# Performance work log

Measured on AMD Instinct MI355X. Metric: run time of the kernel, lower is better.

The kernel has to match this reference:

```python
import jax, jax.numpy as jnp
import numpy as np

N_NODES = 100000
N_EDGES = 1600000
F_IN = 128
F_OUT = 64


def setup_inputs() -> dict:
    key = jax.random.key(0)
    k1, k2, k3, k4 = jax.random.split(key, 4)
    node_features = jax.random.normal(k1, (N_NODES, F_IN), dtype=jnp.float32)
    edge_index = jax.random.randint(k2, (2, N_EDGES), 0, N_NODES, dtype=jnp.int32)
    edge_weight = jax.random.uniform(k3, (N_EDGES,), dtype=jnp.float32)
    W = jax.random.normal(k4, (F_IN, F_OUT), dtype=jnp.float32) * (1.0 / np.sqrt(F_IN))
    b = jnp.zeros((F_OUT,), dtype=jnp.float32)
    return {"node_features": node_features, "edge_index": edge_index,
            "edge_weight": edge_weight, "W": W, "b": b}


def reference(node_features, edge_index, edge_weight, W, b):
    # GCNConv: x' = D^{-1/2} (A + I) D^{-1/2} (X W) + b, edge-weighted.
    n = node_features.shape[0]
    row, col = edge_index[0], edge_index[1]  # source, target
    # add self-loops with weight 1
    loop = jnp.arange(n, dtype=edge_index.dtype)
    row_f = jnp.concatenate([row, loop])
    col_f = jnp.concatenate([col, loop])
    w_f = jnp.concatenate([edge_weight, jnp.ones((n,), edge_weight.dtype)])
    # symmetric normalization
    deg = jax.ops.segment_sum(w_f, col_f, num_segments=n)  # [N]
    dis = jnp.where(deg > 0, jax.lax.rsqrt(deg), 0.0)      # deg^{-1/2}
    norm = dis[row_f] * w_f * dis[col_f]                   # [E+N]
    # transform then scatter-aggregate messages at targets
    xw = node_features @ W                                  # [N, F_OUT]
    msgs = norm[:, None] * xw[row_f]                        # [E+N, F_OUT]
    out = jax.ops.segment_sum(msgs, col_f, num_segments=n)  # [N, F_OUT]
    out = out + b
    # ReLU; dropout(p=0.001) is identity in inference mode
    return jax.nn.relu(out)
```

## Files before the change

kernel.cpp:

```cpp
#include <hip/hip_runtime.h>

#define F_IN 128
#define F_OUT 64
#define LSTR 136
#define EB 4096
#define BSH 8
#define BNODES 256
#define RITER 12

typedef __bf16 bf16x8 __attribute__((ext_vector_type(8)));
typedef float f32x4 __attribute__((ext_vector_type(4)));

__device__ inline ushort f2bf(float f) {
    unsigned u = __float_as_uint(f);
    return (ushort)((u + 0x7fff + ((u >> 16) & 1)) >> 16);
}
__device__ inline float bf2f(ushort u) { return __uint_as_float((unsigned)u << 16); }

__global__ __launch_bounds__(256, 8) void k_hist_gemm(
        const float* __restrict__ X, const float* __restrict__ W,
        const int* __restrict__ colp, unsigned* __restrict__ partials,
        ushort* __restrict__ xwb, int n, int e, int nblk, int nbuck) {
    __shared__ unsigned cnt[512];
    __shared__ ushort Wt[64 * LSTR];
    const int t = threadIdx.x;

    if ((int)blockIdx.x < nblk) {
        const int blk = (int)blockIdx.x;
        cnt[t] = 0; cnt[t + 256] = 0;
        __syncthreads();
        const int base = blk * EB;
        #pragma unroll
        for (int j = 0; j < EB / 256; ++j) {
            int i = base + j * 256 + t;
            if (i < e) atomicAdd(&cnt[(unsigned)colp[i] >> BSH], 1u);
        }
        __syncthreads();
        for (int b = t; b < nbuck; b += 256)
            partials[(size_t)b * nblk + blk] = cnt[b];
        return;
    }

    const int row0 = ((int)blockIdx.x - nblk) * 64;
    const float4* W4 = (const float4*)W;
    #pragma unroll
    for (int i = 0; i < 8; ++i) {
        int idx = t + i * 256;
        float4 v = W4[idx];
        int flat = idx * 4;
        int k = flat >> 6, c = flat & 63;
        Wt[(c + 0) * LSTR + k] = f2bf(v.x);
        Wt[(c + 1) * LSTR + k] = f2bf(v.y);
        Wt[(c + 2) * LSTR + k] = f2bf(v.z);
        Wt[(c + 3) * LSTR + k] = f2bf(v.w);
    }
    const int lane = t & 63, wv_ = t >> 6;
    const int m16 = lane & 15, quad = lane >> 4;
    int arow = row0 + wv_ * 16 + m16;
    if (arow >= n) arow = n - 1;
    const float* xr = X + (long)arow * F_IN;
    __syncthreads();

    f32x4 acc[4] = {{0,0,0,0},{0,0,0,0},{0,0,0,0},{0,0,0,0}};
    #pragma unroll
    for (int kk = 0; kk < 4; ++kk) {
        float4 xa = *(const float4*)(xr + kk * 32 + quad * 8);
        float4 xb = *(const float4*)(xr + kk * 32 + quad * 8 + 4);
        union { ushort us[8]; bf16x8 v; } ua;
        ua.us[0] = f2bf(xa.x); ua.us[1] = f2bf(xa.y);
        ua.us[2] = f2bf(xa.z); ua.us[3] = f2bf(xa.w);
        ua.us[4] = f2bf(xb.x); ua.us[5] = f2bf(xb.y);
        ua.us[6] = f2bf(xb.z); ua.us[7] = f2bf(xb.w);
        #pragma unroll
        for (int nt = 0; nt < 4; ++nt) {
            bf16x8 bb = *(const bf16x8*)&Wt[(nt * 16 + m16) * LSTR + kk * 32 + quad * 8];
            acc[nt] = __builtin_amdgcn_mfma_f32_16x16x32_bf16(ua.v, bb, acc[nt], 0, 0, 0);
        }
    }
    #pragma unroll
    for (int nt = 0; nt < 4; ++nt) {
        #pragma unroll
        for (int reg = 0; reg < 4; ++reg) {
            int gr = row0 + wv_ * 16 + quad * 4 + reg;
            if (gr < n) xwb[(long)gr * F_OUT + nt * 16 + m16] = f2bf(acc[nt][reg]);
        }
    }
}

__global__ __launch_bounds__(512) void k_scan_blocks(
        unsigned* __restrict__ partials, unsigned* __restrict__ totals,
        int nblk, int nbuck) {
    __shared__ unsigned s[512];
    const int b = (int)blockIdx.x, t = threadIdx.x;
    unsigned v = (t < nblk) ? partials[(size_t)b * nblk + t] : 0;
    s[t] = v;
    __syncthreads();
    for (int off = 1; off < 512; off <<= 1) {
        unsigned u = (t >= off) ? s[t - off] : 0;
        __syncthreads();
        s[t] += u;
        __syncthreads();
    }
    if (t < nblk) partials[(size_t)b * nblk + t] = s[t] - v;
    if (t == 511) totals[b] = s[511];
}

__global__ __launch_bounds__(512) void k_scatter(
        const int* __restrict__ ei, const float* __restrict__ ew,
        const unsigned* __restrict__ partials, const unsigned* __restrict__ totals,
        unsigned* __restrict__ sortedA, unsigned char* __restrict__ cl,
        int e, int nblk, int nbuck) {
    __shared__ unsigned srt[EB];
    __shared__ unsigned meta[EB];
    __shared__ unsigned s[512];
    __shared__ unsigned cnt[512];
    __shared__ unsigned ptr[512];
    __shared__ unsigned delta[512];
    const int t = threadIdx.x, blk = (int)blockIdx.x;

    unsigned tv = (t < nbuck) ? totals[t] : 0;
    s[t] = tv; cnt[t] = 0;
    __syncthreads();
    for (int off = 1; off < 512; off <<= 1) {
        unsigned u = (t >= off) ? s[t - off] : 0;
        __syncthreads();
        s[t] += u;
        __syncthreads();
    }
    const unsigned bs = s[t] - tv;

    const int base = blk * EB;
    unsigned cc[EB / 512], rr[EB / 512], ww[EB / 512];
    #pragma unroll
    for (int jj = 0; jj < EB / 512; ++jj) {
        int i = base + jj * 512 + t;
        unsigned c = 0xffffffffu, r = 0, w15 = 0;
        if (i < e) {
            c = (unsigned)ei[e + i];
            r = (unsigned)ei[i];
            unsigned u = __float_as_uint(ew[i]);
            w15 = ((u + 0x7fff + ((u >> 16) & 1)) >> 16) & 0x7fffu;
            atomicAdd(&cnt[c >> BSH], 1u);
        }
        cc[jj] = c; rr[jj] = r; ww[jj] = w15;
    }
    __syncthreads();

    unsigned cv = cnt[t];
    s[t] = cv;
    __syncthreads();
    for (int off = 1; off < 512; off <<= 1) {
        unsigned u = (t >= off) ? s[t - off] : 0;
        __syncthreads();
        s[t] += u;
        __syncthreads();
    }
    const unsigned excl = s[t] - cv;
    ptr[t] = excl;
    delta[t] = bs + ((t < nbuck) ? partials[(size_t)t * nblk + blk] : 0) - excl;
    __syncthreads();

    #pragma unroll
    for (int jj = 0; jj < EB / 512; ++jj) {
        if (cc[jj] != 0xffffffffu) {
            unsigned d = atomicAdd(&ptr[cc[jj] >> BSH], 1u);
            srt[d] = (rr[jj] << 15) | ww[jj];
            meta[d] = cc[jj];
        }
    }
    __syncthreads();

    const int cnum = (e - base < EB) ? (e - base) : EB;
    #pragma unroll
    for (int jj = 0; jj < EB / 512; ++jj) {
        int i = jj * 512 + t;
        if (i < cnum) {
            unsigned c = meta[i];
            unsigned dest = delta[c >> BSH] + (unsigned)i;
            sortedA[dest] = srt[i];
            cl[dest] = (unsigned char)(c & (BNODES - 1));
        }
    }
}

__global__ __launch_bounds__(512) void k_sort_deg(
        unsigned* __restrict__ sortedA, const unsigned char* __restrict__ cl,
        const unsigned* __restrict__ totals, unsigned* __restrict__ nbeg,
        float* __restrict__ dis, int n, int e, int nbuck) {
    __shared__ unsigned s[512];
    __shared__ unsigned cnt[BNODES];
    __shared__ unsigned offs[BNODES];
    __shared__ unsigned ptr[BNODES];
    __shared__ float dl[BNODES];
    __shared__ unsigned Sh, Eh;
    const int b = (int)blockIdx.x, t = threadIdx.x;

    unsigned tv = (t < nbuck) ? totals[t] : 0;
    s[t] = tv;
    __syncthreads();
    for (int off = 1; off < 512; off <<= 1) {
        unsigned u = (t >= off) ? s[t - off] : 0;
        __syncthreads();
        s[t] += u;
        __syncthreads();
    }
    if (t == b) { Sh = s[t] - tv; Eh = s[t]; }
    if (t < BNODES) { cnt[t] = 0; dl[t] = 0.f; }
    __syncthreads();
    const unsigned S = Sh;
    const int seg = (int)(Eh - S);

    unsigned rec[RITER];
    unsigned clp[RITER / 4];
    #pragma unroll
    for (int jj = 0; jj < RITER; ++jj) {
        int j = jj * 512 + t;
        unsigned r = 0, c = 0;
        if (j < seg) {
            r = sortedA[S + j];
            c = cl[S + j];
            atomicAdd(&cnt[c], 1u);
            atomicAdd(&dl[c], __uint_as_float((r & 0x7fffu) << 16));
        }
        rec[jj] = r;
        if ((jj & 3) == 0) clp[jj >> 2] = c;
        else               clp[jj >> 2] |= c << ((jj & 3) * 8);
    }
    __syncthreads();
    if (t < BNODES) offs[t] = cnt[t];
    __syncthreads();
    for (int off = 1; off < BNODES; off <<= 1) {
        unsigned u = (t < BNODES && t >= off) ? offs[t - off] : 0;
        __syncthreads();
        if (t < BNODES) offs[t] += u;
        __syncthreads();
    }
    if (t < BNODES) ptr[t] = offs[t] - cnt[t];
    __syncthreads();
    #pragma unroll
    for (int jj = 0; jj < RITER; ++jj) {
        int j = jj * 512 + t;
        if (j < seg) {
            unsigned c = (clp[jj >> 2] >> ((jj & 3) * 8)) & 0xffu;
            unsigned d = atomicAdd(&ptr[c], 1u);
            sortedA[S + d] = rec[jj];
        }
    }
    if (t < BNODES) {
        int c = b * BNODES + t;
        if (c < n) {
            nbeg[c] = S + (offs[t] - cnt[t]);
            dis[c] = rsqrtf(dl[t] + 1.0f);
        }
    }
    if (b == 0 && t == 0) nbeg[n] = (unsigned)e;
}

__global__ __launch_bounds__(256, 8) void k_gather(
        const unsigned* __restrict__ sortedA, const unsigned* __restrict__ nbeg,
        const float* __restrict__ dis, const ushort* __restrict__ xwb,
        const float* __restrict__ bias, float* __restrict__ out, int n) {
    int node = (int)blockIdx.x * 4 + (threadIdx.x >> 6);
    if (node >= n) return;
    int lane = threadIdx.x & 63, q = lane >> 4, fl = lane & 15;
    unsigned bg = nbeg[node], en = nbeg[node + 1];
    if (en < bg) en = bg;
    int beg = (int)bg, end = (int)en;
    float dc = dis[node];
    float a0 = 0.f, a1 = 0.f, a2 = 0.f, a3 = 0.f;
    if (q == 0) {
        ushort4 xv = *(const ushort4*)(xwb + (long)node * 64 + fl * 4);
        a0 = dc * bf2f(xv.x); a1 = dc * bf2f(xv.y);
        a2 = dc * bf2f(xv.z); a3 = dc * bf2f(xv.w);
    }
    int j = beg + q;
    for (; j + 12 < end; j += 16) {
        unsigned v0 = sortedA[j],     v1 = sortedA[j + 4];
        unsigned v2 = sortedA[j + 8], v3 = sortedA[j + 12];
        int r0 = (int)(v0 >> 15), r1 = (int)(v1 >> 15);
        int r2 = (int)(v2 >> 15), r3 = (int)(v3 >> 15);
        float d0 = dis[r0], d1 = dis[r1], d2 = dis[r2], d3 = dis[r3];
        ushort4 x0 = *(const ushort4*)(xwb + (long)r0 * 64 + fl * 4);
        ushort4 x1 = *(const ushort4*)(xwb + (long)r1 * 64 + fl * 4);
        ushort4 x2 = *(const ushort4*)(xwb + (long)r2 * 64 + fl * 4);
        ushort4 x3 = *(const ushort4*)(xwb + (long)r3 * 64 + fl * 4);
        float w0 = __uint_as_float((v0 & 0x7fffu) << 16) * d0;
        float w1 = __uint_as_float((v1 & 0x7fffu) << 16) * d1;
        float w2 = __uint_as_float((v2 & 0x7fffu) << 16) * d2;
        float w3 = __uint_as_float((v3 & 0x7fffu) << 16) * d3;
        a0 += w0 * bf2f(x0.x) + w1 * bf2f(x1.x) + w2 * bf2f(x2.x) + w3 * bf2f(x3.x);
        a1 += w0 * bf2f(x0.y) + w1 * bf2f(x1.y) + w2 * bf2f(x2.y) + w3 * bf2f(x3.y);
        a2 += w0 * bf2f(x0.z) + w1 * bf2f(x1.z) + w2 * bf2f(x2.z) + w3 * bf2f(x3.z);
        a3 += w0 * bf2f(x0.w) + w1 * bf2f(x1.w) + w2 * bf2f(x2.w) + w3 * bf2f(x3.w);
    }
    for (; j < end; j += 4) {
        unsigned v = sortedA[j];
        int r = (int)(v >> 15);
        float w = __uint_as_float((v & 0x7fffu) << 16) * dis[r];
        ushort4 x = *(const ushort4*)(xwb + (long)r * 64 + fl * 4);
        a0 += w * bf2f(x.x); a1 += w * bf2f(x.y);
        a2 += w * bf2f(x.z); a3 += w * bf2f(x.w);
    }
    a0 += __shfl_xor(a0, 16); a0 += __shfl_xor(a0, 32);
    a1 += __shfl_xor(a1, 16); a1 += __shfl_xor(a1, 32);
    a2 += __shfl_xor(a2, 16); a2 += __shfl_xor(a2, 32);
    a3 += __shfl_xor(a3, 16); a3 += __shfl_xor(a3, 32);
    if (q == 0) {
        float4 bb = ((const float4*)bias)[fl];
        float f0 = dc * a0 + bb.x, f1 = dc * a1 + bb.y;
        float f2 = dc * a2 + bb.z, f3 = dc * a3 + bb.w;
        ((float4*)out)[(long)node * 16 + fl] =
            make_float4(f0 > 0.f ? f0 : 0.f, f1 > 0.f ? f1 : 0.f,
                        f2 > 0.f ? f2 : 0.f, f3 > 0.f ? f3 : 0.f);
    }
}

extern "C" void kernel_launch(void* const* d_in, const int* in_sizes, int n_in,
                              void* d_out, int out_size, void* d_ws, size_t ws_size,
                              hipStream_t stream) {
    const float* X  = (const float*)d_in[0];
    const int*   ei = (const int*)d_in[1];
    const float* ew = (const float*)d_in[2];
    const float* W  = (const float*)d_in[3];
    const float* b  = (const float*)d_in[4];
    float* out = (float*)d_out;

    const int n = in_sizes[0] / F_IN;
    const int e = in_sizes[2];

    const int NBLK  = (e + EB - 1) / EB;
    const int NBUCK = (n + BNODES - 1) / BNODES;
    const int nb_gemm = (n + 63) / 64;

    long p = 0;
    auto alloc = [&](long bytes) { long off = p; p += (bytes + 255) & ~255L; return off; };
    char* ws = (char*)d_ws;
    long o_part   = alloc((long)NBUCK * NBLK * 4);
    long o_tot    = alloc((long)NBUCK * 4);
    long o_sorted = alloc((long)e * 4);
    long o_cl     = alloc((long)e);
    long o_dis    = alloc((long)n * 4);
    long o_nbeg   = alloc((long)(n + 1) * 4);
    long o_xwb    = alloc((long)n * F_OUT * 2);
    unsigned*      partials = (unsigned*)(ws + o_part);
    unsigned*      totals   = (unsigned*)(ws + o_tot);
    unsigned*      sortedA  = (unsigned*)(ws + o_sorted);
    unsigned char* cl       = (unsigned char*)(ws + o_cl);
    float*         dis      = (float*)(ws + o_dis);
    unsigned*      nbeg     = (unsigned*)(ws + o_nbeg);
    ushort*        xwb      = (ushort*)(ws + o_xwb);

    k_hist_gemm<<<NBLK + nb_gemm, 256, 0, stream>>>(X, W, ei + e, partials, xwb,
                                                    n, e, NBLK, NBUCK);
    k_scan_blocks<<<NBUCK, 512, 0, stream>>>(partials, totals, NBLK, NBUCK);
    k_scatter<<<NBLK, 512, 0, stream>>>(ei, ew, partials, totals, sortedA, cl,
                                        e, NBLK, NBUCK);
    k_sort_deg<<<NBUCK, 512, 0, stream>>>(sortedA, cl, totals, nbeg, dis,
                                          n, e, NBUCK);
    k_gather<<<(n + 3) / 4, 256, 0, stream>>>(sortedA, nbeg, dis, xwb, b, out, n);
}
```

Before: 203.2 us.

## Move X@W GEMM blocks from histogram kernel into scatter kernel

```diff
diff --git a/kernel.cpp b/kernel.cpp
--- a/kernel.cpp
+++ b/kernel.cpp
@@ -17,74 +17,22 @@
 }
 __device__ inline float bf2f(ushort u) { return __uint_as_float((unsigned)u << 16); }
 
-__global__ __launch_bounds__(256, 8) void k_hist_gemm(
-        const float* __restrict__ X, const float* __restrict__ W,
+__global__ __launch_bounds__(256) void k_hist(
         const int* __restrict__ colp, unsigned* __restrict__ partials,
-        ushort* __restrict__ xwb, int n, int e, int nblk, int nbuck) {
+        int e, int nblk, int nbuck) {
     __shared__ unsigned cnt[512];
-    __shared__ ushort Wt[64 * LSTR];
-    const int t = threadIdx.x;
-
-    if ((int)blockIdx.x < nblk) {
-        const int blk = (int)blockIdx.x;
-        cnt[t] = 0; cnt[t + 256] = 0;
-        __syncthreads();
-        const int base = blk * EB;
-        #pragma unroll
-        for (int j = 0; j < EB / 256; ++j) {
-            int i = base + j * 256 + t;
-            if (i < e) atomicAdd(&cnt[(unsigned)colp[i] >> BSH], 1u);
-        }
-        __syncthreads();
-        for (int b = t; b < nbuck; b += 256)
-            partials[(size_t)b * nblk + blk] = cnt[b];
-        return;
-    }
-
-    const int row0 = ((int)blockIdx.x - nblk) * 64;
-    const float4* W4 = (const float4*)W;
-    #pragma unroll
-    for (int i = 0; i < 8; ++i) {
-        int idx = t + i * 256;
-        float4 v = W4[idx];
-        int flat = idx * 4;
-        int k = flat >> 6, c = flat & 63;
-        Wt[(c + 0) * LSTR + k] = f2bf(v.x);
-        Wt[(c + 1) * LSTR + k] = f2bf(v.y);
-        Wt[(c + 2) * LSTR + k] = f2bf(v.z);
-        Wt[(c + 3) * LSTR + k] = f2bf(v.w);
-    }
-    const int lane = t & 63, wv_ = t >> 6;
-    const int m16 = lane & 15, quad = lane >> 4;
-    int arow = row0 + wv_ * 16 + m16;
-    if (arow >= n) arow = n - 1;
-    const float* xr = X + (long)arow * F_IN;
-    __syncthreads();
-
-    f32x4 acc[4] = {{0,0,0,0},{0,0,0,0},{0,0,0,0},{0,0,0,0}};
-    #pragma unroll
-    for (int kk = 0; kk < 4; ++kk) {
-        float4 xa = *(const float4*)(xr + kk * 32 + quad * 8);
-        float4 xb = *(const float4*)(xr + kk * 32 + quad * 8 + 4);
-        union { ushort us[8]; bf16x8 v; } ua;
-        ua.us[0] = f2bf(xa.x); ua.us[1] = f2bf(xa.y);
-        ua.us[2] = f2bf(xa.z); ua.us[3] = f2bf(xa.w);
-        ua.us[4] = f2bf(xb.x); ua.us[5] = f2bf(xb.y);
-        ua.us[6] = f2bf(xb.z); ua.us[7] = f2bf(xb.w);
-        #pragma unroll
-        for (int nt = 0; nt < 4; ++nt) {
-            bf16x8 bb = *(const bf16x8*)&Wt[(nt * 16 + m16) * LSTR + kk * 32 + quad * 8];
-            acc[nt] = __builtin_amdgcn_mfma_f32_16x16x32_bf16(ua.v, bb, acc[nt], 0, 0, 0);
-        }
-    }
-    #pragma unroll
-    for (int nt = 0; nt < 4; ++nt) {
-        #pragma unroll
-        for (int reg = 0; reg < 4; ++reg) {
-            int gr = row0 + wv_ * 16 + quad * 4 + reg;
-            if (gr < n) xwb[(long)gr * F_OUT + nt * 16 + m16] = f2bf(acc[nt][reg]);
-        }
-    }
+    const int t = threadIdx.x, blk = (int)blockIdx.x;
+    cnt[t] = 0; cnt[t + 256] = 0;
+    __syncthreads();
+    const int base = blk * EB;
+    #pragma unroll
+    for (int j = 0; j < EB / 256; ++j) {
+        int i = base + j * 256 + t;
+        if (i < e) atomicAdd(&cnt[(unsigned)colp[i] >> BSH], 1u);
+    }
+    __syncthreads();
+    for (int b = t; b < nbuck; b += 256)
+        partials[(size_t)b * nblk + blk] = cnt[b];
 }
 
 __global__ __launch_bounds__(512) void k_scan_blocks(
@@ -105,29 +53,85 @@
     if (t == 511) totals[b] = s[511];
 }
 
-__global__ __launch_bounds__(512) void k_scatter(
+__global__ __launch_bounds__(512) void k_scatter_gemm(
+        const float* __restrict__ X, const float* __restrict__ W,
         const int* __restrict__ ei, const float* __restrict__ ew,
         const unsigned* __restrict__ partials, const unsigned* __restrict__ totals,
         unsigned* __restrict__ sortedA, unsigned char* __restrict__ cl,
-        int e, int nblk, int nbuck) {
-    __shared__ unsigned srt[EB];
-    __shared__ unsigned meta[EB];
-    __shared__ unsigned s[512];
-    __shared__ unsigned cnt[512];
-    __shared__ unsigned ptr[512];
-    __shared__ unsigned delta[512];
-    const int t = threadIdx.x, blk = (int)blockIdx.x;
-
+        ushort* __restrict__ xwb, int n, int e, int nblk, int nbuck) {
+    __shared__ union SM {
+        struct {
+            unsigned srt[EB];
+            unsigned meta[EB];
+            unsigned s[512];
+            unsigned cnt[512];
+            unsigned ptr[512];
+            unsigned delta[512];
+        } sc;
+        ushort Wt[64 * LSTR];
+    } sm;
+    const int t = threadIdx.x;
+
+    if ((int)blockIdx.x >= nblk) {
+        ushort* Wt = sm.Wt;
+        const int row0 = ((int)blockIdx.x - nblk) * 128;
+        const float4* W4 = (const float4*)W;
+        #pragma unroll
+        for (int i = 0; i < 4; ++i) {
+            int idx = t + i * 512;
+            float4 v = W4[idx];
+            int flat = idx * 4;
+            int k = flat >> 6, c = flat & 63;
+            Wt[(c + 0) * LSTR + k] = f2bf(v.x);
+            Wt[(c + 1) * LSTR + k] = f2bf(v.y);
+            Wt[(c + 2) * LSTR + k] = f2bf(v.z);
+            Wt[(c + 3) * LSTR + k] = f2bf(v.w);
+        }
+        const int lane = t & 63, wv_ = t >> 6;
+        const int m16 = lane & 15, quad = lane >> 4;
+        int arow = row0 + wv_ * 16 + m16;
+        if (arow >= n) arow = n - 1;
+        const float* xr = X + (long)arow * F_IN;
+        __syncthreads();
+
+        f32x4 acc[4] = {{0,0,0,0},{0,0,0,0},{0,0,0,0},{0,0,0,0}};
+        #pragma unroll
+        for (int kk = 0; kk < 4; ++kk) {
+            float4 xa = *(const float4*)(xr + kk * 32 + quad * 8);
+            float4 xb = *(const float4*)(xr + kk * 32 + quad * 8 + 4);
+            union { ushort us[8]; bf16x8 v; } ua;
+            ua.us[0] = f2bf(xa.x); ua.us[1] = f2bf(xa.y);
+            ua.us[2] = f2bf(xa.z); ua.us[3] = f2bf(xa.w);
+            ua.us[4] = f2bf(xb.x); ua.us[5] = f2bf(xb.y);
+            ua.us[6] = f2bf(xb.z); ua.us[7] = f2bf(xb.w);
+            #pragma unroll
+            for (int nt = 0; nt < 4; ++nt) {
+                bf16x8 bb = *(const bf16x8*)&Wt[(nt * 16 + m16) * LSTR + kk * 32 + quad * 8];
+                acc[nt] = __builtin_amdgcn_mfma_f32_16x16x32_bf16(ua.v, bb, acc[nt], 0, 0, 0);
+            }
+        }
+        #pragma unroll
+        for (int nt = 0; nt < 4; ++nt) {
+            #pragma unroll
+            for (int reg = 0; reg < 4; ++reg) {
+                int gr = row0 + wv_ * 16 + quad * 4 + reg;
+                if (gr < n) xwb[(long)gr * F_OUT + nt * 16 + m16] = f2bf(acc[nt][reg]);
+            }
+        }
+        return;
+    }
+
+    const int blk = (int)blockIdx.x;
     unsigned tv = (t < nbuck) ? totals[t] : 0;
-    s[t] = tv; cnt[t] = 0;
+    sm.sc.s[t] = tv; sm.sc.cnt[t] = 0;
     __syncthreads();
     for (int off = 1; off < 512; off <<= 1) {
-        unsigned u = (t >= off) ? s[t - off] : 0;
-        __syncthreads();
-        s[t] += u;
-        __syncthreads();
-    }
-    const unsigned bs = s[t] - tv;
+        unsigned u = (t >= off) ? sm.sc.s[t - off] : 0;
+        __syncthreads();
+        sm.sc.s[t] += u;
+        __syncthreads();
+    }
+    const unsigned bs = sm.sc.s[t] - tv;
 
     const int base = blk * EB;
     unsigned cc[EB / 512], rr[EB / 512], ww[EB / 512];
@@ -140,32 +144,32 @@
             r = (unsigned)ei[i];
             unsigned u = __float_as_uint(ew[i]);
             w15 = ((u + 0x7fff + ((u >> 16) & 1)) >> 16) & 0x7fffu;
-            atomicAdd(&cnt[c >> BSH], 1u);
+            atomicAdd(&sm.sc.cnt[c >> BSH], 1u);
         }
         cc[jj] = c; rr[jj] = r; ww[jj] = w15;
     }
     __syncthreads();
 
-    unsigned cv = cnt[t];
-    s[t] = cv;
+    unsigned cv = sm.sc.cnt[t];
+    sm.sc.s[t] = cv;
     __syncthreads();
     for (int off = 1; off < 512; off <<= 1) {
-        unsigned u = (t >= off) ? s[t - off] : 0;
-        __syncthreads();
-        s[t] += u;
-        __syncthreads();
-    }
-    const unsigned excl = s[t] - cv;
-    ptr[t] = excl;
-    delta[t] = bs + ((t < nbuck) ? partials[(size_t)t * nblk + blk] : 0) - excl;
+        unsigned u = (t >= off) ? sm.sc.s[t - off] : 0;
+        __syncthreads();
+        sm.sc.s[t] += u;
+        __syncthreads();
+    }
+    const unsigned excl = sm.sc.s[t] - cv;
+    sm.sc.ptr[t] = excl;
+    sm.sc.delta[t] = bs + ((t < nbuck) ? partials[(size_t)t * nblk + blk] : 0) - excl;
     __syncthreads();
 
     #pragma unroll
     for (int jj = 0; jj < EB / 512; ++jj) {
         if (cc[jj] != 0xffffffffu) {
-            unsigned d = atomicAdd(&ptr[cc[jj] >> BSH], 1u);
-            srt[d] = (rr[jj] << 15) | ww[jj];
-            meta[d] = cc[jj];
+            unsigned d = atomicAdd(&sm.sc.ptr[cc[jj] >> BSH], 1u);
+            sm.sc.srt[d] = (rr[jj] << 15) | ww[jj];
+            sm.sc.meta[d] = cc[jj];
         }
     }
     __syncthreads();
@@ -175,9 +179,9 @@
     for (int jj = 0; jj < EB / 512; ++jj) {
         int i = jj * 512 + t;
         if (i < cnum) {
-            unsigned c = meta[i];
-            unsigned dest = delta[c >> BSH] + (unsigned)i;
-            sortedA[dest] = srt[i];
+            unsigned c = sm.sc.meta[i];
+            unsigned dest = sm.sc.delta[c >> BSH] + (unsigned)i;
+            sortedA[dest] = sm.sc.srt[i];
             cl[dest] = (unsigned char)(c & (BNODES - 1));
         }
     }
@@ -273,10 +277,11 @@
         a0 = dc * bf2f(xv.x); a1 = dc * bf2f(xv.y);
         a2 = dc * bf2f(xv.z); a3 = dc * bf2f(xv.w);
     }
-    int j = beg + q;
-    for (; j + 12 < end; j += 16) {
-        unsigned v0 = sortedA[j],     v1 = sortedA[j + 4];
-        unsigned v2 = sortedA[j + 8], v3 = sortedA[j + 12];
+    for (int j = beg + q; j < end; j += 16) {
+        bool m1 = j + 4 < end, m2 = j + 8 < end, m3 = j + 12 < end;
+        int j1 = m1 ? j + 4 : j, j2 = m2 ? j + 8 : j, j3 = m3 ? j + 12 : j;
+        unsigned v0 = sortedA[j],  v1 = sortedA[j1];
+        unsigned v2 = sortedA[j2], v3 = sortedA[j3];
         int r0 = (int)(v0 >> 15), r1 = (int)(v1 >> 15);
         int r2 = (int)(v2 >> 15), r3 = (int)(v3 >> 15);
         float d0 = dis[r0], d1 = dis[r1], d2 = dis[r2], d3 = dis[r3];
@@ -285,21 +290,13 @@
         ushort4 x2 = *(const ushort4*)(xwb + (long)r2 * 64 + fl * 4);
         ushort4 x3 = *(const ushort4*)(xwb + (long)r3 * 64 + fl * 4);
         float w0 = __uint_as_float((v0 & 0x7fffu) << 16) * d0;
-        float w1 = __uint_as_float((v1 & 0x7fffu) << 16) * d1;
-        float w2 = __uint_as_float((v2 & 0x7fffu) << 16) * d2;
-        float w3 = __uint_as_float((v3 & 0x7fffu) << 16) * d3;
+        float w1 = m1 ? __uint_as_float((v1 & 0x7fffu) << 16) * d1 : 0.f;
+        float w2 = m2 ? __uint_as_float((v2 & 0x7fffu) << 16) * d2 : 0.f;
+        float w3 = m3 ? __uint_as_float((v3 & 0x7fffu) << 16) * d3 : 0.f;
         a0 += w0 * bf2f(x0.x) + w1 * bf2f(x1.x) + w2 * bf2f(x2.x) + w3 * bf2f(x3.x);
         a1 += w0 * bf2f(x0.y) + w1 * bf2f(x1.y) + w2 * bf2f(x2.y) + w3 * bf2f(x3.y);
         a2 += w0 * bf2f(x0.z) + w1 * bf2f(x1.z) + w2 * bf2f(x2.z) + w3 * bf2f(x3.z);
         a3 += w0 * bf2f(x0.w) + w1 * bf2f(x1.w) + w2 * bf2f(x2.w) + w3 * bf2f(x3.w);
-    }
-    for (; j < end; j += 4) {
-        unsigned v = sortedA[j];
-        int r = (int)(v >> 15);
-        float w = __uint_as_float((v & 0x7fffu) << 16) * dis[r];
-        ushort4 x = *(const ushort4*)(xwb + (long)r * 64 + fl * 4);
-        a0 += w * bf2f(x.x); a1 += w * bf2f(x.y);
-        a2 += w * bf2f(x.z); a3 += w * bf2f(x.w);
     }
     a0 += __shfl_xor(a0, 16); a0 += __shfl_xor(a0, 32);
     a1 += __shfl_xor(a1, 16); a1 += __shfl_xor(a1, 32);
@@ -330,7 +327,7 @@
 
     const int NBLK  = (e + EB - 1) / EB;
     const int NBUCK = (n + BNODES - 1) / BNODES;
-    const int nb_gemm = (n + 63) / 64;
+    const int nb_gemm = (n + 127) / 128;
 
     long p = 0;
     auto alloc = [&](long bytes) { long off = p; p += (bytes + 255) & ~255L; return off; };
@@ -350,11 +347,11 @@
     unsigned*      nbeg     = (unsigned*)(ws + o_nbeg);
     ushort*        xwb      = (ushort*)(ws + o_xwb);
 
-    k_hist_gemm<<<NBLK + nb_gemm, 256, 0, stream>>>(X, W, ei + e, partials, xwb,
-                                                    n, e, NBLK, NBUCK);
+    k_hist<<<NBLK, 256, 0, stream>>>(ei + e, partials, e, NBLK, NBUCK);
     k_scan_blocks<<<NBUCK, 512, 0, stream>>>(partials, totals, NBLK, NBUCK);
-    k_scatter<<<NBLK, 512, 0, stream>>>(ei, ew, partials, totals, sortedA, cl,
-                                        e, NBLK, NBUCK);
+    k_scatter_gemm<<<NBLK + nb_gemm, 512, 0, stream>>>(X, W, ei, ew, partials,
+                                                       totals, sortedA, cl, xwb,
+                                                       n, e, NBLK, NBUCK);
     k_sort_deg<<<NBUCK, 512, 0, stream>>>(sortedA, cl, totals, nbeg, dis,
                                           n, e, NBUCK);
     k_gather<<<(n + 3) / 4, 256, 0, stream>>>(sortedA, nbeg, dis, xwb, b, out, n);
```

New measurement: 198.1 us. 2.5% less time.
